# Performance work log

Hardware: AMD Instinct MI355X
Metric: run time of the kernel (lower is better)

## Reference

```python
import jax, jax.numpy as jnp
import numpy as np

BS, N, M, D = 8, 2048, 64, 1024
N_WAY, N_SHOT = 64, 5


def setup_inputs() -> dict:
    key = jax.random.key(0)
    k1, k2, k3, k4, k5 = jax.random.split(key, 5)
    return {
        "prototypes": jax.random.normal(k1, (BS, M, D), dtype=jnp.float32),
        "masktypes": jax.random.uniform(k2, (BS, M, D), dtype=jnp.float32),
        "query": jax.random.normal(k3, (BS, N, D), dtype=jnp.float32),
        "support": jax.random.normal(k4, (BS, N_WAY * N_SHOT, D), dtype=jnp.float32),
        "support_labels": jax.random.randint(k5, (BS, N_WAY * N_SHOT), 0, N_WAY, dtype=jnp.int64),
        "scale": jnp.ones((1,), dtype=jnp.float32),
        "n_way": N_WAY,
        "n_shot": N_SHOT,
    }


def reference(prototypes, masktypes, query, support, support_labels, scale, n_way, n_shot):
    # Masked squared Euclidean distance:
    #   logits[b,n,m] = sum_d (mask[b,m,d] * (query[b,n,d] - proto[b,m,d]))^2
    # Expanded via the GEMM trick to avoid the (bs,n,m,d) intermediate:
    #   = sum_d mask^2 q^2 - 2 sum_d q (mask^2 p) + sum_d (mask p)^2
    dims = prototypes.shape[-1]
    mask2 = masktypes * masktypes                       # [b,m,d]
    q_term = jnp.einsum('bnd,bmd->bnm', query * query, mask2)
    cross = jnp.einsum('bnd,bmd->bnm', query, mask2 * prototypes)
    mp = masktypes * prototypes                         # [b,m,d]
    p_term = jnp.sum(mp * mp, axis=-1)[:, None, :]      # [b,1,m]
    logits = (q_term - 2.0 * cross + p_term) / dims     # normalize=True
    return scale * logits
```

## Files before the change

kernel.cpp:

```cpp
#include <hip/hip_runtime.h>

#define BSZ 8
#define NQ 2048
#define MP 64
#define DD 1024
#define K2ALL 2048
#define NSTEP 64

typedef __bf16 bf16x8 __attribute__((ext_vector_type(8)));
typedef float f32x4 __attribute__((ext_vector_type(4)));
typedef unsigned short us8 __attribute__((ext_vector_type(8)));

union FragU { us8 u; bf16x8 b; };

__device__ __forceinline__ unsigned short f2bf(float f) {
    union { float f; unsigned int u; } v; v.f = f;
    unsigned int u = v.u;
    return (unsigned short)((u + 0x7FFFu + ((u >> 16) & 1u)) >> 16);
}

__global__ __launch_bounds__(256) void pack_kernel(
    const float* __restrict__ proto,
    const float* __restrict__ mask,
    unsigned short* __restrict__ Pf,
    float* __restrict__ Pterm)
{
    const int row = blockIdx.x;
    const int m = row & 63;
    const int b = row >> 6;
    const int t = threadIdx.x;

    const float4 mk = *(const float4*)(mask  + (size_t)row * DD + 4 * t);
    const float4 pr = *(const float4*)(proto + (size_t)row * DD + 4 * t);

    const float m2x = mk.x * mk.x, m2y = mk.y * mk.y,
                m2z = mk.z * mk.z, m2w = mk.w * mk.w;
    const float ax = mk.x * pr.x, ay = mk.y * pr.y,
                az = mk.z * pr.z, aw = mk.w * pr.w;
    float pacc = ax * ax + ay * ay + az * az + aw * aw;

    us8 o;
    o[0] = f2bf(m2x); o[1] = f2bf(-2.f * m2x * pr.x);
    o[2] = f2bf(m2y); o[3] = f2bf(-2.f * m2y * pr.y);
    o[4] = f2bf(m2z); o[5] = f2bf(-2.f * m2z * pr.z);
    o[6] = f2bf(m2w); o[7] = f2bf(-2.f * m2w * pr.w);

    const int mt   = m >> 4;
    const int s    = t >> 2;
    const int lane = (t & 3) * 16 + (m & 15);
    const size_t idx = ((((size_t)(b * 4 + mt)) * 64 + s) * 64 + lane) * 8;
    *(us8*)(Pf + idx) = o;

    __shared__ float red[4];
    #pragma unroll
    for (int off = 32; off > 0; off >>= 1)
        pacc += __shfl_down(pacc, off, 64);
    const int lane64 = t & 63, w = t >> 6;
    if (lane64 == 0) red[w] = pacc;
    __syncthreads();
    if (t == 0) Pterm[row] = red[0] + red[1] + red[2] + red[3];
}

__global__ __launch_bounds__(256, 1) void proto_main_kernel(
    const float* __restrict__ query,
    const unsigned short* __restrict__ Pf,
    const float* __restrict__ Pterm,
    const float* __restrict__ scale,
    float* __restrict__ out)
{
    const int tid  = threadIdx.x;
    const int bid  = blockIdx.x;
    const int b    = bid & 7;
    const int wid  = tid >> 6;
    const int lane = tid & 63;
    const int lrow = lane & 15;
    const int quad = lane >> 4;
    const int n0   = (bid >> 3) * 64 + wid * 16;

    const float* aptr = query + ((size_t)b * NQ + n0 + lrow) * DD + 4 * quad;
    const unsigned short* bp = Pf + ((size_t)(b * 4)) * 64 * 512 + (size_t)lane * 8;

    float4 aq[8];
    #pragma unroll
    for (int i = 0; i < 8; ++i)
        aq[i] = *(const float4*)(aptr + 16 * i);

    bf16x8 bq[4][4];
    #pragma unroll
    for (int s = 0; s < 4; ++s)
        #pragma unroll
        for (int mt = 0; mt < 4; ++mt)
            bq[s][mt] = *(const bf16x8*)(bp + (size_t)mt * 32768 + (size_t)s * 512);

    const float sc = scale[0] * (1.0f / (float)DD);
    float pt[4];
    #pragma unroll
    for (int mt = 0; mt < 4; ++mt)
        pt[mt] = Pterm[b * MP + 16 * mt + lrow];

    f32x4 acc[4];
    acc[0] = acc[1] = acc[2] = acc[3] = (f32x4){0.f, 0.f, 0.f, 0.f};

    for (int g = 0; g < NSTEP; g += 8) {
        #pragma unroll
        for (int j = 0; j < 8; ++j) {
            const int s = g + j;
            const float4 q = aq[s & 7];
            if (s + 8 < NSTEP)
                aq[s & 7] = *(const float4*)(aptr + 16 * (s + 8));

            FragU af;
            af.u[0] = f2bf(q.x * q.x); af.u[1] = f2bf(q.x);
            af.u[2] = f2bf(q.y * q.y); af.u[3] = f2bf(q.y);
            af.u[4] = f2bf(q.z * q.z); af.u[5] = f2bf(q.z);
            af.u[6] = f2bf(q.w * q.w); af.u[7] = f2bf(q.w);
            const bf16x8 a = af.b;

            #pragma unroll
            for (int mt = 0; mt < 4; ++mt) {
                const bf16x8 bb = bq[s & 3][mt];
                if (s + 4 < NSTEP)
                    bq[s & 3][mt] = *(const bf16x8*)(
                        bp + (size_t)mt * 32768 + (size_t)(s + 4) * 512);
                acc[mt] = __builtin_amdgcn_mfma_f32_16x16x32_bf16(a, bb, acc[mt], 0, 0, 0);
            }
        }
    }

    #pragma unroll
    for (int mt = 0; mt < 4; ++mt) {
        const size_t ob =
            ((size_t)b * NQ + (size_t)(n0 + quad * 4)) * MP + 16 * mt + lrow;
        #pragma unroll
        for (int r = 0; r < 4; ++r)
            out[ob + (size_t)r * MP] = (acc[mt][r] + pt[mt]) * sc;
    }
}

extern "C" void kernel_launch(void* const* d_in, const int* in_sizes, int n_in,
                              void* d_out, int out_size, void* d_ws, size_t ws_size,
                              hipStream_t stream) {
    (void)in_sizes; (void)n_in; (void)ws_size; (void)out_size;
    const float* proto = (const float*)d_in[0];
    const float* mask  = (const float*)d_in[1];
    const float* query = (const float*)d_in[2];
    const float* scale = (const float*)d_in[5];
    float* out = (float*)d_out;

    unsigned short* Pf = (unsigned short*)d_ws;
    float* Pterm = (float*)((char*)d_ws + (size_t)BSZ * MP * K2ALL * 2);

    pack_kernel<<<dim3(BSZ * MP), dim3(256), 0, stream>>>(proto, mask, Pf, Pterm);
    proto_main_kernel<<<dim3(256), dim3(256), 0, stream>>>(
        query, Pf, Pterm, scale, out);
}
```

Measured before the change: 137.7 us.

## Stage query and packed prototypes through double-buffered LDS with async loads

The main kernel now loads query tiles and packed prototype fragments through LDS with global_load_lds async copies, double-buffered across 16 K-steps and separated by block barriers. Each block covers 32 query rows instead of 64, so twice as many blocks are launched, and launch bounds now allow 2 blocks per CU. All four waves share the B fragments from LDS, and an XOR swizzle on the query layout avoids bank conflicts. This aims to raise occupancy and overlap memory with MFMA work, at the cost of LDS traffic and a barrier per step.

Measured after the change: 136.3 us. About the same (-1.0%).

```diff
diff --git a/kernel.cpp b/kernel.cpp
--- a/kernel.cpp
+++ b/kernel.cpp
@@ -1,22 +1,36 @@
 #include <hip/hip_runtime.h>
+#include <hip/hip_bf16.h>
 
 #define BSZ 8
 #define NQ 2048
 #define MP 64
 #define DD 1024
 #define K2ALL 2048
-#define NSTEP 64
+#define BN 32
+#define BK 64
+#define KT 16
+#define NTILES (NQ / BN)
 
 typedef __bf16 bf16x8 __attribute__((ext_vector_type(8)));
 typedef float f32x4 __attribute__((ext_vector_type(4)));
 typedef unsigned short us8 __attribute__((ext_vector_type(8)));
 
-union FragU { us8 u; bf16x8 b; };
-
 __device__ __forceinline__ unsigned short f2bf(float f) {
     union { float f; unsigned int u; } v; v.f = f;
     unsigned int u = v.u;
     return (unsigned short)((u + 0x7FFFu + ((u >> 16) & 1u)) >> 16);
+}
+
+__device__ __forceinline__ void async_ld16(const void* g, void* l) {
+    __builtin_amdgcn_global_load_lds(
+        (const __attribute__((address_space(1))) unsigned int*)g,
+        (__attribute__((address_space(3))) unsigned int*)l, 16, 0, 0);
+}
+
+__device__ __forceinline__ unsigned int pk2(float a, float b) {
+    union { __hip_bfloat162 h; unsigned int u; } c;
+    c.h = __float22bfloat162_rn(make_float2(a, b));
+    return c.u;
 }
 
 __global__ __launch_bounds__(256) void pack_kernel(
@@ -61,36 +75,33 @@
     if (t == 0) Pterm[row] = red[0] + red[1] + red[2] + red[3];
 }
 
-__global__ __launch_bounds__(256, 1) void proto_main_kernel(
+__global__ __launch_bounds__(256, 2) void proto_main_kernel(
     const float* __restrict__ query,
     const unsigned short* __restrict__ Pf,
     const float* __restrict__ Pterm,
     const float* __restrict__ scale,
     float* __restrict__ out)
 {
-    const int tid  = threadIdx.x;
-    const int bid  = blockIdx.x;
-    const int b    = bid & 7;
+    __shared__ float          Qsh[2][BN * BK];
+    __shared__ unsigned short Bsh[2][16 * 512];
+
+    const int tid = threadIdx.x;
+    const int bid = blockIdx.x;
+    const int b   = bid & 7;
+    const int n0  = (bid >> 3) * BN;
+
+    const int lane = tid & 63;
     const int wid  = tid >> 6;
-    const int lane = tid & 63;
     const int lrow = lane & 15;
     const int quad = lane >> 4;
-    const int n0   = (bid >> 3) * 64 + wid * 16;
 
-    const float* aptr = query + ((size_t)b * NQ + n0 + lrow) * DD + 4 * quad;
-    const unsigned short* bp = Pf + ((size_t)(b * 4)) * 64 * 512 + (size_t)lane * 8;
+    const int row0 = (wid * 2 + 0) * 4 + quad;
+    const int row1 = (wid * 2 + 1) * 4 + quad;
+    const float* qsrc0 = query + ((size_t)b * NQ + n0 + row0) * DD + 4 * (lrow ^ (row0 & 15));
+    const float* qsrc1 = query + ((size_t)b * NQ + n0 + row1) * DD + 4 * (lrow ^ (row1 & 15));
 
-    float4 aq[8];
-    #pragma unroll
-    for (int i = 0; i < 8; ++i)
-        aq[i] = *(const float4*)(aptr + 16 * i);
-
-    bf16x8 bq[4][4];
-    #pragma unroll
-    for (int s = 0; s < 4; ++s)
-        #pragma unroll
-        for (int mt = 0; mt < 4; ++mt)
-            bq[s][mt] = *(const bf16x8*)(bp + (size_t)mt * 32768 + (size_t)s * 512);
+    const unsigned short* bsrc =
+        Pf + (((size_t)(b * 4 + wid)) * 64) * 512 + (size_t)lane * 8;
 
     const float sc = scale[0] * (1.0f / (float)DD);
     float pt[4];
@@ -98,42 +109,70 @@
     for (int mt = 0; mt < 4; ++mt)
         pt[mt] = Pterm[b * MP + 16 * mt + lrow];
 
-    f32x4 acc[4];
-    acc[0] = acc[1] = acc[2] = acc[3] = (f32x4){0.f, 0.f, 0.f, 0.f};
+    f32x4 acc[2][4];
+    #pragma unroll
+    for (int nt = 0; nt < 2; ++nt)
+        #pragma unroll
+        for (int mt = 0; mt < 4; ++mt)
+            acc[nt][mt] = (f32x4){0.f, 0.f, 0.f, 0.f};
 
-    for (int g = 0; g < NSTEP; g += 8) {
+    {
+        async_ld16(qsrc0, &Qsh[0][(wid * 2 + 0) * 256]);
+        async_ld16(qsrc1, &Qsh[0][(wid * 2 + 1) * 256]);
         #pragma unroll
-        for (int j = 0; j < 8; ++j) {
-            const int s = g + j;
-            const float4 q = aq[s & 7];
-            if (s + 8 < NSTEP)
-                aq[s & 7] = *(const float4*)(aptr + 16 * (s + 8));
+        for (int sl = 0; sl < 4; ++sl)
+            async_ld16(bsrc + (size_t)sl * 512, &Bsh[0][(wid * 4 + sl) * 512]);
+    }
 
-            FragU af;
-            af.u[0] = f2bf(q.x * q.x); af.u[1] = f2bf(q.x);
-            af.u[2] = f2bf(q.y * q.y); af.u[3] = f2bf(q.y);
-            af.u[4] = f2bf(q.z * q.z); af.u[5] = f2bf(q.z);
-            af.u[6] = f2bf(q.w * q.w); af.u[7] = f2bf(q.w);
-            const bf16x8 a = af.b;
+    for (int kt = 0; kt < KT; ++kt) {
+        const int c = kt & 1;
+        __syncthreads();
 
+        if (kt + 1 < KT) {
+            const int nc = c ^ 1;
+            async_ld16(qsrc0 + (size_t)(kt + 1) * BK, &Qsh[nc][(wid * 2 + 0) * 256]);
+            async_ld16(qsrc1 + (size_t)(kt + 1) * BK, &Qsh[nc][(wid * 2 + 1) * 256]);
+            #pragma unroll
+            for (int sl = 0; sl < 4; ++sl)
+                async_ld16(bsrc + (size_t)(4 * (kt + 1) + sl) * 512,
+                           &Bsh[nc][(wid * 4 + sl) * 512]);
+        }
+
+        #pragma unroll
+        for (int sl = 0; sl < 4; ++sl) {
+            bf16x8 afr[2];
+            #pragma unroll
+            for (int nt = 0; nt < 2; ++nt) {
+                const int row = 16 * nt + lrow;
+                const int dgx = (4 * sl + quad) ^ lrow;
+                const float4 q = *(const float4*)&Qsh[c][(row * 16 + dgx) * 4];
+                union { uint4 u; bf16x8 b; } cv;
+                cv.u.x = pk2(q.x * q.x, q.x);
+                cv.u.y = pk2(q.y * q.y, q.y);
+                cv.u.z = pk2(q.z * q.z, q.z);
+                cv.u.w = pk2(q.w * q.w, q.w);
+                afr[nt] = cv.b;
+            }
             #pragma unroll
             for (int mt = 0; mt < 4; ++mt) {
-                const bf16x8 bb = bq[s & 3][mt];
-                if (s + 4 < NSTEP)
-                    bq[s & 3][mt] = *(const bf16x8*)(
-                        bp + (size_t)mt * 32768 + (size_t)(s + 4) * 512);
-                acc[mt] = __builtin_amdgcn_mfma_f32_16x16x32_bf16(a, bb, acc[mt], 0, 0, 0);
+                const bf16x8 bb =
+                    *(const bf16x8*)&Bsh[c][(mt * 4 + sl) * 512 + lane * 8];
+                acc[0][mt] = __builtin_amdgcn_mfma_f32_16x16x32_bf16(afr[0], bb, acc[0][mt], 0, 0, 0);
+                acc[1][mt] = __builtin_amdgcn_mfma_f32_16x16x32_bf16(afr[1], bb, acc[1][mt], 0, 0, 0);
             }
         }
     }
 
     #pragma unroll
-    for (int mt = 0; mt < 4; ++mt) {
-        const size_t ob =
-            ((size_t)b * NQ + (size_t)(n0 + quad * 4)) * MP + 16 * mt + lrow;
+    for (int nt = 0; nt < 2; ++nt) {
         #pragma unroll
-        for (int r = 0; r < 4; ++r)
-            out[ob + (size_t)r * MP] = (acc[mt][r] + pt[mt]) * sc;
+        for (int mt = 0; mt < 4; ++mt) {
+            const size_t ob =
+                ((size_t)b * NQ + (size_t)(n0 + 16 * nt + quad * 4)) * MP + 16 * mt + lrow;
+            #pragma unroll
+            for (int r = 0; r < 4; ++r)
+                out[ob + (size_t)r * MP] = (acc[nt][mt][r] + pt[mt]) * sc;
+        }
     }
 }
 
@@ -151,6 +190,6 @@
     float* Pterm = (float*)((char*)d_ws + (size_t)BSZ * MP * K2ALL * 2);
 
     pack_kernel<<<dim3(BSZ * MP), dim3(256), 0, stream>>>(proto, mask, Pf, Pterm);
-    proto_main_kernel<<<dim3(256), dim3(256), 0, stream>>>(
+    proto_main_kernel<<<dim3(BSZ * NTILES), dim3(256), 0, stream>>>(
         query, Pf, Pterm, scale, out);
 }
```
